# Kernel optimization log

Hardware: AMD Instinct MI355X
Metric: run time of the kernel (lower is better)

Reference implementation:

```python
import jax, jax.numpy as jnp
import numpy as np

# Production-scale dims (see shape_source)
B, H, W, C = 8, 64, 64, 256
KH, KW = 3, 3
BASES = 16
FILTERS = 256


def setup_inputs() -> dict:
    key = jax.random.key(0)
    k1, k2, k3, k4 = jax.random.split(key, 4)
    x = jax.random.normal(k1, (B, H, W, C), dtype=jnp.float32)
    # P: channel-mixing matrix [C, C] (initialized to identity in build, then assigned)
    P = jax.random.normal(k2, (C, C), dtype=jnp.float32) * 0.05
    # Q: per-channel basis kernels [C, kh, kw, bases]
    Q = jax.random.normal(k3, (C, KH, KW, BASES), dtype=jnp.float32) * 0.1
    # S: basis-combination weights [C, bases, filters]
    S = jax.random.normal(k4, (C, BASES, FILTERS), dtype=jnp.float32) * 0.05
    return {"x": x, "P": P, "Q": Q, "S": S}


def reference(x, P, Q, S):
    # --- Step 1: channel mixing (the vectorized_map over calculate_J) ---
    # J[o] = sum_c x[..., c] * P[o, c]  ->  one GEMM over channels
    mixed = jnp.einsum('bhwc,oc->bhwo', x, P)  # [B,H,W,C]

    C_ = P.shape[0]
    kh, kw, bases = Q.shape[1], Q.shape[2], Q.shape[3]

    # --- Step 2: per-channel conv with `bases` basis kernels (the map_fn loop) ---
    # Expressed as ONE grouped (depthwise-style) conv: group c produces outputs
    # [c*bases : (c+1)*bases], matching kernel flatten order (c, b).
    rhs = jnp.transpose(Q, (1, 2, 0, 3)).reshape(kh, kw, 1, C_ * bases)  # HWIO
    dw = jax.lax.conv_general_dilated(
        mixed, rhs, window_strides=(1, 1), padding='VALID',
        dimension_numbers=('NHWC', 'HWIO', 'NHWC'),
        feature_group_count=C_,
    )  # [B, H-kh+1, W-kw+1, C*bases], channel index k = c*bases + b

    b, h, w, _ = dw.shape
    # tau in the original: [B, h, w, bases, C]
    tau = dw.reshape(b, h, w, C_, bases).transpose(0, 1, 2, 4, 3)

    # --- Step 3: basis-weighted combination (the vectorized_map over calculate_O) ---
    # Original flattens tau row-major over (bases, C) and S[:, :, f] row-major over
    # (C, bases), then does an elementwise dot over the flat axis. Replicate exactly.
    Tflat = tau.reshape(b, h, w, bases * C_)          # flat index k = b_idx*C + c
    Sflat = S.reshape(C_ * bases, S.shape[-1])        # flat index k = c*bases + b_idx
    O = jnp.einsum('bhwk,kf->bhwf', Tflat, Sflat)     # [B, h, w, filters]
    return O
```

## Files before the change

### kernel.cpp

```cpp
#include <hip/hip_runtime.h>
#include <hip/hip_bf16.h>

typedef __attribute__((ext_vector_type(4))) float f32x4;
typedef __attribute__((ext_vector_type(8))) short bf16x8;
typedef __attribute__((ext_vector_type(4))) unsigned int u32x4;

#define M_TOT 30752

__device__ __forceinline__ unsigned short f2bf(float f) {
  unsigned int u = __float_as_uint(f);
  u = u + 0x7FFF + ((u >> 16) & 1);
  return (unsigned short)(u >> 16);
}

__device__ __forceinline__ void gload16(const void* g, void* l) {
  __builtin_amdgcn_global_load_lds((const __attribute__((address_space(1))) unsigned int*)g,
                                   (__attribute__((address_space(3))) unsigned int*)l,
                                   16, 0, 0);
}

#define CVT_PK(dst, lo, hi) \
  asm("v_cvt_pk_bf16_f32 %0, %1, %2" : "=v"(dst) : "v"(lo), "v"(hi))

__global__ __launch_bounds__(256) void keff_k(const float* __restrict__ Q,
                                              const float* __restrict__ S,
                                              float* __restrict__ Keff) {
  const int o = blockIdx.x;
  const int t = threadIdx.x;
  float s[16];
  const float* sp = S + (o >> 4) * 4096 + (o & 15) * 256 + t;
#pragma unroll
  for (int bi = 0; bi < 16; ++bi) s[bi] = sp[bi * 65536];
  const float* qp = Q + o * 144;
#pragma unroll
  for (int kk = 0; kk < 9; ++kk) {
    float a = 0.f;
#pragma unroll
    for (int bi = 0; bi < 16; ++bi) a = fmaf(qp[kk * 16 + bi], s[bi], a);
    Keff[(o * 9 + kk) * 256 + t] = a;
  }
}

__global__ __launch_bounds__(256) void k2t_k(const float* __restrict__ P,
                                             const float* __restrict__ Keff,
                                             unsigned short* __restrict__ K2t) {
  const int kk = blockIdx.x >> 6;
  const int f0 = (blockIdx.x & 63) * 4;
  const int ci = threadIdx.x;
  float acc[4] = {0.f, 0.f, 0.f, 0.f};
#pragma unroll 8
  for (int o = 0; o < 256; ++o) {
    float pv = P[o * 256 + ci];
    const float* ke = Keff + (o * 9 + kk) * 256 + f0;
    acc[0] = fmaf(pv, ke[0], acc[0]);
    acc[1] = fmaf(pv, ke[1], acc[1]);
    acc[2] = fmaf(pv, ke[2], acc[2]);
    acc[3] = fmaf(pv, ke[3], acc[3]);
  }
#pragma unroll
  for (int j = 0; j < 4; ++j)
    K2t[kk * 65536 + (f0 + j) * 256 + ci] = f2bf(acc[j]);
}

__global__ __launch_bounds__(256, 2) void conv_gemm(const float* __restrict__ x,
                                                    const unsigned short* __restrict__ K2t,
                                                    float* __restrict__ out) {
  __shared__ __attribute__((aligned(16))) char smem[65536];

  const int tid = threadIdx.x;
  const int lane = tid & 63;
  const int wid = tid >> 6;
  const int sk = wid >> 1;
  const int wn = wid & 1;

  const int wgid = (blockIdx.x & 7) * 61 + (blockIdx.x >> 3);
  if (wgid >= 482) return;
  const int mt = wgid >> 1;
  const int nt = wgid & 1;
  const int m0 = mt * 128;
  const int n0 = nt * 128;

  const int rl = lane & 15;
  const int kg = lane >> 4;

  const int s_src = ((tid & 3) ^ ((tid >> 3) & 3)) * 8;
  int gA0, gA1;
  {
    int m = m0 + (tid >> 2); if (m >= M_TOT) m = M_TOT - 1;
    int b = m / 3844; int rem = m - b * 3844;
    int h = rem / 62; int w = rem - h * 62;
    gA0 = ((b * 64 + h) * 64 + w) * 256 + s_src;
    m = m0 + (tid >> 2) + 64; if (m >= M_TOT) m = M_TOT - 1;
    b = m / 3844; rem = m - b * 3844;
    h = rem / 62; w = rem - h * 62;
    gA1 = ((b * 64 + h) * 64 + w) * 256 + s_src;
  }
  const int fB0 = (n0 + (tid >> 2)) * 256 + s_src;
  const int fB1 = (n0 + (tid >> 2) + 64) * 256 + s_src;

  f32x4 zero = {0.f, 0.f, 0.f, 0.f};
  f32x4 acc[8][4];
#pragma unroll
  for (int i = 0; i < 8; ++i)
#pragma unroll
    for (int j = 0; j < 4; ++j) acc[i][j] = zero;

  f32x4 av[8];

  const int slotr = (kg ^ ((rl >> 1) & 3)) * 16;
  const int aoff = sk * 8192 + rl * 64 + slotr;
  const int boff = 16384 + sk * 8192 + (wn * 64 + rl) * 64 + slotr;

#define A_LOAD(t)                                                              \
  {                                                                            \
    int kk_ = (t) >> 2, cb_ = (t) & 3;                                         \
    int kh_ = kk_ / 3, kw_ = kk_ - kh_ * 3;                                    \
    int offA_ = kh_ * 16384 + kw_ * 256 + cb_ * 64;                            \
    const f32x4* p0 = (const f32x4*)(x + gA0 + offA_);                         \
    const f32x4* p1 = (const f32x4*)(x + gA1 + offA_);                         \
    av[0] = p0[0]; av[1] = p0[1];                                              \
    av[2] = p1[0]; av[3] = p1[1];                                              \
    av[4] = p0[8]; av[5] = p0[9];                        \
    av[6] = p1[8]; av[7] = p1[9];                                              \
  }

#define STAGE_B(t, base)                                                       \
  {                                                                            \
    int kk_ = (t) >> 2, cb_ = (t) & 3;                                         \
    int offB_ = kk_ * 65536 + cb_ * 64;                                        \
    unsigned short* bB = (unsigned short*)((char*)(base) + 16384);             \
    gload16(K2t + offB_ + fB0,      bB + tid * 8);                             \
    gload16(K2t + offB_ + fB1,      bB + (tid + 256) * 8);                     \
    gload16(K2t + offB_ + fB0 + 32, bB + (tid + 512) * 8);                     \
    gload16(K2t + offB_ + fB1 + 32, bB + (tid + 768) * 8);                     \
  }

#define A_WRITE(base)                                                          \
  {                                                                            \
    unsigned short* bA = (unsigned short*)(base);                              \
    _Pragma("unroll")                                                          \
    for (int q = 0; q < 4; ++q) {                                              \
      unsigned int w0, w1, w2, w3;                                             \
      CVT_PK(w0, av[2 * q][0], av[2 * q][1]);                                  \
      CVT_PK(w1, av[2 * q][2], av[2 * q][3]);                                  \
      CVT_PK(w2, av[2 * q + 1][0], av[2 * q + 1][1]);                          \
      CVT_PK(w3, av[2 * q + 1][2], av[2 * q + 1][3]);                          \
      u32x4 w = {w0, w1, w2, w3};                                              \
      *(u32x4*)(bA + (tid + 256 * q) * 8) = w;              \
    }                                                                          \
  }

  A_LOAD(0);
  __builtin_amdgcn_sched_barrier(0);
  STAGE_B(0, smem);
  asm volatile("s_waitcnt vmcnt(4)" ::: "memory");
  __builtin_amdgcn_sched_barrier(0);
  A_WRITE(smem);

  for (int t = 0; t < 36; ++t) {
    char* cur = smem + (t & 1) * 32768;
    char* nxt = smem + ((t + 1) & 1) * 32768;

    if (t < 35) {
      A_LOAD(t + 1);
      __builtin_amdgcn_sched_barrier(0);
      STAGE_B(t + 1, nxt);
      asm volatile("s_waitcnt vmcnt(12)" ::: "memory");
    } else {
      asm volatile("s_waitcnt vmcnt(0)" ::: "memory");
    }
    asm volatile("s_waitcnt lgkmcnt(0)" ::: "memory");
    __builtin_amdgcn_sched_barrier(0);
    __builtin_amdgcn_s_barrier();
    __builtin_amdgcn_sched_barrier(0);

    bf16x8 bfr[4];
#pragma unroll
    for (int ni = 0; ni < 4; ++ni)
      bfr[ni] = *(const bf16x8*)(cur + boff + ni * 1024);
    bf16x8 a0 = *(const bf16x8*)(cur + aoff);
    bf16x8 a1 = *(const bf16x8*)(cur + aoff + 1024);
#pragma unroll
    for (int j = 0; j < 4; ++j) {
      bf16x8 a2, a3;
      if (j < 3) {
        a2 = *(const bf16x8*)(cur + aoff + (2 * j + 2) * 1024);
        a3 = *(const bf16x8*)(cur + aoff + (2 * j + 3) * 1024);
      }
      __builtin_amdgcn_s_setprio(1);
#pragma unroll
      for (int ni = 0; ni < 4; ++ni)
        acc[2 * j][ni] = __builtin_amdgcn_mfma_f32_16x16x32_bf16(
            a0, bfr[ni], acc[2 * j][ni], 0, 0, 0);
#pragma unroll
      for (int ni = 0; ni < 4; ++ni)
        acc[2 * j + 1][ni] = __builtin_amdgcn_mfma_f32_16x16x32_bf16(
            a1, bfr[ni], acc[2 * j + 1][ni], 0, 0, 0);
      __builtin_amdgcn_s_setprio(0);
      a0 = a2; a1 = a3;
    }

    if (t < 35) {
      asm volatile("s_waitcnt vmcnt(4)" ::: "memory");
      __builtin_amdgcn_sched_barrier(0);
      A_WRITE(nxt);
    }
  }

  float* red = (float*)smem;
  __syncthreads();
  if (sk == 1) {
#pragma unroll
    for (int mi = 0; mi < 8; ++mi)
#pragma unroll
      for (int ni = 0; ni < 4; ++ni)
        *(f32x4*)((char*)red + (((wn * 8 + mi) * 4 + ni) * 64 + lane) * 16) =
            acc[mi][ni];
  }
  __syncthreads();
  if (sk == 0) {
#pragma unroll
    for (int mi = 0; mi < 8; ++mi) {
      int mb = m0 + mi * 16 + kg * 4;
#pragma unroll
      for (int ni = 0; ni < 4; ++ni) {
        f32x4 o = *(f32x4*)((char*)red + (((wn * 8 + mi) * 4 + ni) * 64 + lane) * 16);
        o += acc[mi][ni];
        int f = n0 + wn * 64 + ni * 16 + rl;
#pragma unroll
        for (int r = 0; r < 4; ++r) {
          int m = mb + r;
          if (m < M_TOT) out[m * 256 + f] = o[r];
        }
      }
    }
  }
#undef A_LOAD
#undef STAGE_B
#undef A_WRITE
}

extern "C" void kernel_launch(void* const* d_in, const int* in_sizes, int n_in,
                              void* d_out, int out_size, void* d_ws, size_t ws_size,
                              hipStream_t stream) {
  const float* x = (const float*)d_in[0];
  const float* P = (const float*)d_in[1];
  const float* Q = (const float*)d_in[2];
  const float* S = (const float*)d_in[3];
  float* out = (float*)d_out;

  char* ws = (char*)d_ws;
  unsigned short* K2t  = (unsigned short*)ws;
  float*          Keff = (float*)(ws + 1179648);

  keff_k<<<256, 256, 0, stream>>>(Q, S, Keff);
  k2t_k<<<576, 256, 0, stream>>>(P, Keff, K2t);
  conv_gemm<<<488, 256, 0, stream>>>(x, K2t, out);
}
```

Before: 83.98 us.

## Tile conv GEMM by output row pairs with shared input halo in LDS

The conv GEMM now assigns each workgroup two output rows (124 sites) of one image and loads the 4x64 input-row window for a 64-channel slice into LDS once. All nine kernel taps are then read from that window instead of re-gathering x from global memory per tap. Loop order changes to channel-block outer, tap inner, with only B double-buffered per step. Keff and K2t precompute are fused into one kernel that builds the Keff slice in LDS, removing a launch and a workspace round trip. The trade-off is lower M-tile utilisation (124 of 128 rows used) and a slightly larger grid.

Measured after the change: 101.8 us. +21.2%, slower.

```diff
diff --git a/kernel.cpp b/kernel.cpp
--- a/kernel.cpp
+++ b/kernel.cpp
@@ -22,40 +22,38 @@
 #define CVT_PK(dst, lo, hi) \
   asm("v_cvt_pk_bf16_f32 %0, %1, %2" : "=v"(dst) : "v"(lo), "v"(hi))
 
-__global__ __launch_bounds__(256) void keff_k(const float* __restrict__ Q,
-                                              const float* __restrict__ S,
-                                              float* __restrict__ Keff) {
-  const int o = blockIdx.x;
+__global__ __launch_bounds__(256) void k2t_f(const float* __restrict__ P,
+                                             const float* __restrict__ Q,
+                                             const float* __restrict__ S,
+                                             unsigned short* __restrict__ K2t) {
+  __shared__ float ldsK[256 * 4];
+  const int kk = blockIdx.x / 64;
+  const int f0 = (blockIdx.x & 63) * 4;
   const int t = threadIdx.x;
-  float s[16];
-  const float* sp = S + (o >> 4) * 4096 + (o & 15) * 256 + t;
-#pragma unroll
-  for (int bi = 0; bi < 16; ++bi) s[bi] = sp[bi * 65536];
-  const float* qp = Q + o * 144;
-#pragma unroll
-  for (int kk = 0; kk < 9; ++kk) {
-    float a = 0.f;
-#pragma unroll
-    for (int bi = 0; bi < 16; ++bi) a = fmaf(qp[kk * 16 + bi], s[bi], a);
-    Keff[(o * 9 + kk) * 256 + t] = a;
-  }
-}
-
-__global__ __launch_bounds__(256) void k2t_k(const float* __restrict__ P,
-                                             const float* __restrict__ Keff,
-                                             unsigned short* __restrict__ K2t) {
-  const int kk = blockIdx.x >> 6;
-  const int f0 = (blockIdx.x & 63) * 4;
-  const int ci = threadIdx.x;
+  {
+    float k0 = 0.f, k1 = 0.f, k2 = 0.f, k3 = 0.f;
+    const float* qp = Q + t * 144 + kk * 16;
+    const float* sp = S + (t >> 4) * 4096 + (t & 15) * 256 + f0;
+#pragma unroll
+    for (int bi = 0; bi < 16; ++bi) {
+      float qv = qp[bi];
+      const float* s4 = sp + bi * 65536;
+      k0 = fmaf(qv, s4[0], k0); k1 = fmaf(qv, s4[1], k1);
+      k2 = fmaf(qv, s4[2], k2); k3 = fmaf(qv, s4[3], k3);
+    }
+    ldsK[t * 4 + 0] = k0; ldsK[t * 4 + 1] = k1;
+    ldsK[t * 4 + 2] = k2; ldsK[t * 4 + 3] = k3;
+  }
+  __syncthreads();
+  const int ci = t;
   float acc[4] = {0.f, 0.f, 0.f, 0.f};
 #pragma unroll 8
   for (int o = 0; o < 256; ++o) {
     float pv = P[o * 256 + ci];
-    const float* ke = Keff + (o * 9 + kk) * 256 + f0;
-    acc[0] = fmaf(pv, ke[0], acc[0]);
-    acc[1] = fmaf(pv, ke[1], acc[1]);
-    acc[2] = fmaf(pv, ke[2], acc[2]);
-    acc[3] = fmaf(pv, ke[3], acc[3]);
+    acc[0] = fmaf(pv, ldsK[o * 4 + 0], acc[0]);
+    acc[1] = fmaf(pv, ldsK[o * 4 + 1], acc[1]);
+    acc[2] = fmaf(pv, ldsK[o * 4 + 2], acc[2]);
+    acc[3] = fmaf(pv, ldsK[o * 4 + 3], acc[3]);
   }
 #pragma unroll
   for (int j = 0; j < 4; ++j)
@@ -73,30 +71,36 @@
   const int sk = wid >> 1;
   const int wn = wid & 1;
 
-  const int wgid = (blockIdx.x & 7) * 61 + (blockIdx.x >> 3);
-  if (wgid >= 482) return;
+  const int wgid = (blockIdx.x & 7) * 62 + (blockIdx.x >> 3);
   const int mt = wgid >> 1;
   const int nt = wgid & 1;
-  const int m0 = mt * 128;
+  const int bimg = mt / 31;
+  const int rr2 = mt - bimg * 31;
+  const int m_base = bimg * 3844 + rr2 * 124;
+  const int xb0 = (bimg * 64 + rr2 * 2) * 16384;
   const int n0 = nt * 128;
 
   const int rl = lane & 15;
   const int kg = lane >> 4;
 
-  const int s_src = ((tid & 3) ^ ((tid >> 3) & 3)) * 8;
-  int gA0, gA1;
-  {
-    int m = m0 + (tid >> 2); if (m >= M_TOT) m = M_TOT - 1;
-    int b = m / 3844; int rem = m - b * 3844;
-    int h = rem / 62; int w = rem - h * 62;
-    gA0 = ((b * 64 + h) * 64 + w) * 256 + s_src;
-    m = m0 + (tid >> 2) + 64; if (m >= M_TOT) m = M_TOT - 1;
-    b = m / 3844; rem = m - b * 3844;
-    h = rem / 62; w = rem - h * 62;
-    gA1 = ((b * 64 + h) * 64 + w) * 256 + s_src;
-  }
-  const int fB0 = (n0 + (tid >> 2)) * 256 + s_src;
-  const int fB1 = (n0 + (tid >> 2) + 64) * 256 + s_src;
+  const int s_srcB = ((tid & 3) ^ ((tid >> 3) & 3)) * 8;
+  const int fB0 = (n0 + (tid >> 2)) * 256 + s_srcB;
+  const int fB1 = (n0 + (tid >> 2) + 64) * 256 + s_srcB;
+
+  const int wsite0 = tid >> 3;
+  const int wd = tid & 7;
+
+  int s8[8];
+#pragma unroll
+  for (int mi = 0; mi < 8; ++mi) {
+    int lr = mi * 16 + rl; if (lr > 123) lr = 123;
+    int ho = (lr >= 62) ? 1 : 0;
+    s8[mi] = ho * 64 + (lr - ho * 62);
+  }
+  const int csl = sk * 4 + kg;
+
+  const int slotrB = (kg ^ ((rl >> 1) & 3)) * 16;
+  const int boffR = sk * 8192 + (wn * 64 + rl) * 64 + slotrB;
 
   f32x4 zero = {0.f, 0.f, 0.f, 0.f};
   f32x4 acc[8][4];
@@ -105,110 +109,99 @@
 #pragma unroll
     for (int j = 0; j < 4; ++j) acc[i][j] = zero;
 
-  f32x4 av[8];
-
-  const int slotr = (kg ^ ((rl >> 1) & 3)) * 16;
-  const int aoff = sk * 8192 + rl * 64 + slotr;
-  const int boff = 16384 + sk * 8192 + (wn * 64 + rl) * 64 + slotr;
-
-#define A_LOAD(t)                                                              \
+  f32x4 wv[16];
+
+#define STAGE_B(u, base)                                                       \
   {                                                                            \
-    int kk_ = (t) >> 2, cb_ = (t) & 3;                                         \
-    int kh_ = kk_ / 3, kw_ = kk_ - kh_ * 3;                                    \
-    int offA_ = kh_ * 16384 + kw_ * 256 + cb_ * 64;                            \
-    const f32x4* p0 = (const f32x4*)(x + gA0 + offA_);                         \
-    const f32x4* p1 = (const f32x4*)(x + gA1 + offA_);                         \
-    av[0] = p0[0]; av[1] = p0[1];                                              \
-    av[2] = p1[0]; av[3] = p1[1];                                              \
-    av[4] = p0[8]; av[5] = p0[9];                        \
-    av[6] = p1[8]; av[7] = p1[9];                                              \
-  }
-
-#define STAGE_B(t, base)                                                       \
+    int kku = (u) % 9, cbu = (u) / 9;                                          \
+    int offB = kku * 65536 + cbu * 64;                                         \
+    unsigned short* bB = (unsigned short*)(base);                              \
+    gload16(K2t + offB + fB0,      bB + tid * 8);                              \
+    gload16(K2t + offB + fB1,      bB + (tid + 256) * 8);                      \
+    gload16(K2t + offB + fB0 + 32, bB + (tid + 512) * 8);                      \
+    gload16(K2t + offB + fB1 + 32, bB + (tid + 768) * 8);                      \
+  }
+
+#define W_LOAD(J0, cbn)                                                        \
   {                                                                            \
-    int kk_ = (t) >> 2, cb_ = (t) & 3;                                         \
-    int offB_ = kk_ * 65536 + cb_ * 64;                                        \
-    unsigned short* bB = (unsigned short*)((char*)(base) + 16384);             \
-    gload16(K2t + offB_ + fB0,      bB + tid * 8);                             \
-    gload16(K2t + offB_ + fB1,      bB + (tid + 256) * 8);                     \
-    gload16(K2t + offB_ + fB0 + 32, bB + (tid + 512) * 8);                     \
-    gload16(K2t + offB_ + fB1 + 32, bB + (tid + 768) * 8);                     \
-  }
-
-#define A_WRITE(base)                                                          \
+    _Pragma("unroll")                                                          \
+    for (int j = (J0); j < (J0) + 4; ++j) {                                    \
+      const f32x4* p = (const f32x4*)(x + xb0 + (wsite0 + 32 * j) * 256 +      \
+                                      (cbn) * 64 + wd * 8);                    \
+      wv[2 * j] = p[0]; wv[2 * j + 1] = p[1];                                  \
+    }                                                                          \
+  }
+
+#define W_WRITE()                                                              \
   {                                                                            \
-    unsigned short* bA = (unsigned short*)(base);                              \
     _Pragma("unroll")                                                          \
-    for (int q = 0; q < 4; ++q) {                                              \
-      unsigned int w0, w1, w2, w3;                                             \
-      CVT_PK(w0, av[2 * q][0], av[2 * q][1]);                                  \
-      CVT_PK(w1, av[2 * q][2], av[2 * q][3]);                                  \
-      CVT_PK(w2, av[2 * q + 1][0], av[2 * q + 1][1]);                          \
-      CVT_PK(w3, av[2 * q + 1][2], av[2 * q + 1][3]);                          \
-      u32x4 w = {w0, w1, w2, w3};                                              \
-      *(u32x4*)(bA + (tid + 256 * q) * 8) = w;              \
+    for (int j = 0; j < 8; ++j) {                                              \
+      int st = wsite0 + 32 * j;                                                \
+      unsigned int c0, c1, c2, c3;                                             \
+      CVT_PK(c0, wv[2 * j][0], wv[2 * j][1]);                                  \
+      CVT_PK(c1, wv[2 * j][2], wv[2 * j][3]);                                  \
+      CVT_PK(c2, wv[2 * j + 1][0], wv[2 * j + 1][1]);                          \
+      CVT_PK(c3, wv[2 * j + 1][2], wv[2 * j + 1][3]);                          \
+      u32x4 q = {c0, c1, c2, c3};                                              \
+      *(u32x4*)(smem + st * 128 + ((wd ^ (st & 7)) << 4)) = q;                 \
     }                                                                          \
   }
 
-  A_LOAD(0);
-  __builtin_amdgcn_sched_barrier(0);
-  STAGE_B(0, smem);
+  W_LOAD(0, 0); W_LOAD(4, 0);
+  STAGE_B(0, smem + 32768);
   asm volatile("s_waitcnt vmcnt(4)" ::: "memory");
   __builtin_amdgcn_sched_barrier(0);
-  A_WRITE(smem);
-
-  for (int t = 0; t < 36; ++t) {
-    char* cur = smem + (t & 1) * 32768;
-    char* nxt = smem + ((t + 1) & 1) * 32768;
-
-    if (t < 35) {
-      A_LOAD(t + 1);
+  W_WRITE();
+
+#pragma unroll
+  for (int cb = 0; cb < 4; ++cb) {
+#pragma unroll
+    for (int kk = 0; kk < 9; ++kk) {
+      const int t = cb * 9 + kk;
+      const int kh = kk / 3, kw = kk - kh * 3;
+      char* curB = smem + 32768 + (t & 1) * 16384;
+      if (t < 35) STAGE_B(t + 1, smem + 32768 + ((t + 1) & 1) * 16384);
+      if (t == 35)              asm volatile("s_waitcnt vmcnt(0)" ::: "memory");
+      else if (kk == 7 && cb < 3) asm volatile("s_waitcnt vmcnt(12)" ::: "memory");
+      else                      asm volatile("s_waitcnt vmcnt(4)" ::: "memory");
+      if (kk == 0) asm volatile("s_waitcnt lgkmcnt(0)" ::: "memory");
       __builtin_amdgcn_sched_barrier(0);
-      STAGE_B(t + 1, nxt);
-      asm volatile("s_waitcnt vmcnt(12)" ::: "memory");
-    } else {
-      asm volatile("s_waitcnt vmcnt(0)" ::: "memory");
-    }
-    asm volatile("s_waitcnt lgkmcnt(0)" ::: "memory");
-    __builtin_amdgcn_sched_barrier(0);
-    __builtin_amdgcn_s_barrier();
-    __builtin_amdgcn_sched_barrier(0);
-
-    bf16x8 bfr[4];
-#pragma unroll
-    for (int ni = 0; ni < 4; ++ni)
-      bfr[ni] = *(const bf16x8*)(cur + boff + ni * 1024);
-    bf16x8 a0 = *(const bf16x8*)(cur + aoff);
-    bf16x8 a1 = *(const bf16x8*)(cur + aoff + 1024);
-#pragma unroll
-    for (int j = 0; j < 4; ++j) {
-      bf16x8 a2, a3;
-      if (j < 3) {
-        a2 = *(const bf16x8*)(cur + aoff + (2 * j + 2) * 1024);
-        a3 = *(const bf16x8*)(cur + aoff + (2 * j + 3) * 1024);
+      __builtin_amdgcn_s_barrier();
+      __builtin_amdgcn_sched_barrier(0);
+
+      bf16x8 bfr[4];
+#pragma unroll
+      for (int ni = 0; ni < 4; ++ni)
+        bfr[ni] = *(const bf16x8*)(curB + boffR + ni * 1024);
+      bf16x8 af[8];
+#pragma unroll
+      for (int mi = 0; mi < 8; ++mi) {
+        int st = s8[mi] + kh * 64 + kw;
+        af[mi] = *(const bf16x8*)(smem + st * 128 + ((csl ^ (st & 7)) << 4));
       }
       __builtin_amdgcn_s_setprio(1);
 #pragma unroll
-      for (int ni = 0; ni < 4; ++ni)
-        acc[2 * j][ni] = __builtin_amdgcn_mfma_f32_16x16x32_bf16(
-            a0, bfr[ni], acc[2 * j][ni], 0, 0, 0);
-#pragma unroll
-      for (int ni = 0; ni < 4; ++ni)
-        acc[2 * j + 1][ni] = __builtin_amdgcn_mfma_f32_16x16x32_bf16(
-            a1, bfr[ni], acc[2 * j + 1][ni], 0, 0, 0);
+      for (int mi = 0; mi < 8; ++mi)
+#pragma unroll
+        for (int ni = 0; ni < 4; ++ni)
+          acc[mi][ni] = __builtin_amdgcn_mfma_f32_16x16x32_bf16(
+              af[mi], bfr[ni], acc[mi][ni], 0, 0, 0);
       __builtin_amdgcn_s_setprio(0);
-      a0 = a2; a1 = a3;
+
+      if (kk == 6 && cb < 3) { W_LOAD(0, cb + 1); }
+      if (kk == 7 && cb < 3) { W_LOAD(4, cb + 1); }
+      if (kk == 8 && cb < 3) {
+        __builtin_amdgcn_sched_barrier(0);
+        __builtin_amdgcn_s_barrier();
+        __builtin_amdgcn_sched_barrier(0);
+        W_WRITE();
+      }
     }
-
-    if (t < 35) {
-      asm volatile("s_waitcnt vmcnt(4)" ::: "memory");
-      __builtin_amdgcn_sched_barrier(0);
-      A_WRITE(nxt);
-    }
-  }
+  }
+
+  __syncthreads();
 
   float* red = (float*)smem;
-  __syncthreads();
   if (sk == 1) {
 #pragma unroll
     for (int mi = 0; mi < 8; ++mi)
@@ -221,7 +214,6 @@
   if (sk == 0) {
 #pragma unroll
     for (int mi = 0; mi < 8; ++mi) {
-      int mb = m0 + mi * 16 + kg * 4;
 #pragma unroll
       for (int ni = 0; ni < 4; ++ni) {
         f32x4 o = *(f32x4*)((char*)red + (((wn * 8 + mi) * 4 + ni) * 64 + lane) * 16);
@@ -229,15 +221,15 @@
         int f = n0 + wn * 64 + ni * 16 + rl;
 #pragma unroll
         for (int r = 0; r < 4; ++r) {
-          int m = mb + r;
-          if (m < M_TOT) out[m * 256 + f] = o[r];
+          int lrow = mi * 16 + kg * 4 + r;
+          if (lrow < 124) out[(m_base + lrow) * 256 + f] = o[r];
         }
       }
     }
   }
-#undef A_LOAD
 #undef STAGE_B
-#undef A_WRITE
+#undef W_LOAD
+#undef W_WRITE
 }
 
 extern "C" void kernel_launch(void* const* d_in, const int* in_sizes, int n_in,
@@ -249,11 +241,8 @@
   const float* S = (const float*)d_in[3];
   float* out = (float*)d_out;
 
-  char* ws = (char*)d_ws;
-  unsigned short* K2t  = (unsigned short*)ws;
-  float*          Keff = (float*)(ws + 1179648);
-
-  keff_k<<<256, 256, 0, stream>>>(Q, S, Keff);
-  k2t_k<<<576, 256, 0, stream>>>(P, Keff, K2t);
-  conv_gemm<<<488, 256, 0, stream>>>(x, K2t, out);
-}
+  unsigned short* K2t = (unsigned short*)d_ws;
+
+  k2t_f<<<576, 256, 0, stream>>>(P, Q, S, K2t);
+  conv_gemm<<<496, 256, 0, stream>>>(x, K2t, out);
+}
```
